# Performance work log

Measured on AMD Instinct MI355X. Metric: run time of the kernel, lower is better.

Reference implementation:

```python
import jax, jax.numpy as jnp
import numpy as np

N_LAYERS = 4


def setup_inputs() -> dict:
    key = jax.random.key(0)
    k1, k2 = jax.random.split(key)
    data = jax.random.normal(k1, (100000, 512), dtype=jnp.float32)
    codebooks = jax.random.normal(k2, (N_LAYERS, 1024, 512), dtype=jnp.float32) * 0.1
    return {"data": data, "codebooks": codebooks}


def _nearest(residual, cb):
    # squared euclidean distances [N, K]; argmin identical to cdist argmin
    x2 = jnp.sum(residual * residual, axis=1, keepdims=True)        # [N,1]
    c2 = jnp.sum(cb * cb, axis=1)[None, :]                          # [1,K]
    d2 = x2 + c2 - 2.0 * (residual @ cb.T)                          # [N,K]
    return jnp.argmin(d2, axis=1)


def reference(data, codebooks):
    """encode (iterative residual quantization) then decode. Returns (codes, reconstructed)."""
    residual = data
    codes = []
    recon = jnp.zeros_like(data)
    for l in range(N_LAYERS):  # small fixed layer count, sequential dependency
        cb = codebooks[l]                       # [K,F]
        idx = _nearest(residual, cb)            # [N]
        q = cb[idx]                             # gather [N,F]
        residual = residual - q
        recon = recon + q
        codes.append(idx)
    codes = jnp.stack(codes, axis=1).astype(jnp.int64)  # [N, n_layers]
    return codes, recon
```

## Files before the change

kernel.cpp:

```cpp
#include <hip/hip_runtime.h>
#include <hip/hip_bf16.h>
#include <math.h>

#define NL 4
#define KC 1024
#define FD 512
#define MT 32
#define BLK 512
#define HBLK 256
#define RS 516
#define PPS 132
#define NCAND 6

typedef __attribute__((ext_vector_type(8))) short short8;
typedef __attribute__((ext_vector_type(4))) float f32x4;

__device__ __forceinline__ short bf16c(float x) {
  __hip_bfloat16 h = __float2bfloat16(x);
  return *reinterpret_cast<short*>(&h);
}

__device__ __forceinline__ float np_chunk_partial(const float* p, int l16) {
  float pm[8];
#pragma unroll
  for (int m = 0; m < 8; m++) {
    float v = p[m * 16 + l16];
    pm[m] = __fmul_rn(v, v);
  }
  float a = __fadd_rn(__fadd_rn(pm[0], pm[1]), __fadd_rn(pm[2], pm[3]));
  float b = __fadd_rn(__fadd_rn(pm[4], pm[5]), __fadd_rn(pm[6], pm[7]));
  return __fadd_rn(a, b);
}

__global__ __launch_bounds__(HBLK) void c2_kernel(const float* __restrict__ cb,
                                                  float* __restrict__ c2) {
  int wid  = (blockIdx.x * HBLK + threadIdx.x) >> 6;
  int lane = threadIdx.x & 63;
  if (wid >= NL * KC) return;
  const float* row = cb + (size_t)wid * FD;
  int chunk = lane >> 4, l16 = lane & 15;
  float part = np_chunk_partial(row + chunk * 128, l16);
  part = __fadd_rn(part, __shfl_xor(part, 8));
  part = __fadd_rn(part, __shfl_xor(part, 4));
  part = __fadd_rn(part, __shfl_xor(part, 2));
  part = __fadd_rn(part, __shfl_xor(part, 1));
  float s1 = __fadd_rn(part, __shfl_xor(part, 16));
  float s  = __fadd_rn(s1, __shfl_xor(s1, 32));
  if (lane == 0) c2[wid] = s;
}

__global__ __launch_bounds__(HBLK) void swz_kernel(const float* __restrict__ cb,
                                                   short* __restrict__ cbw) {
  int g = blockIdx.x * HBLK + threadIdx.x;
  int w = g >> 6, lane = g & 63;
  if (w >= NL * 16 * 64) return;
  int l = w >> 10, c = (w >> 6) & 15, T = w & 63;
  int kidx = T * 16 + (lane & 15);
  int f0   = c * 32 + ((lane >> 4) << 3);
  const float* src = cb + (((size_t)l * KC + kidx) * FD + f0);
  short8 v;
#pragma unroll
  for (int j = 0; j < 8; j++) v[j] = bf16c(src[j]);
  *(short8*)(cbw + (size_t)w * 512 + lane * 8) = v;
}

#define INS(dval, kval) do {                                              \
    float _d = (dval); int _k = (kval);                                   \
    _Pragma("unroll")                                                     \
    for (int _j = 0; _j < NCAND; _j++) {                                  \
      bool _b = (_d < cd[_j]) || (_d == cd[_j] && _k < ck[_j]);           \
      if (_b) { float _td = cd[_j]; cd[_j] = _d; _d = _td;                \
                int   _tk = ck[_j]; ck[_j] = _k; _k = _tk; }              \
    }                                                                     \
  } while (0)

__global__ __launch_bounds__(BLK, 2) void rq_kernel(
    const float* __restrict__ data, const float* __restrict__ cb,
    const float* __restrict__ c2g, const short* __restrict__ cbw,
    float* __restrict__ codes_out, float* __restrict__ recon_out, int N) {
  __shared__ float resid[MT * RS];
  __shared__ float pool_d[MT * PPS];
  __shared__ int   pool_k[MT * PPS];
  __shared__ float mrg_d[MT * 24];
  __shared__ int   mrg_k[MT * 24];
  __shared__ float sh_part[MT * 64];
  __shared__ float sh_x2[MT];
  __shared__ float sc_d[MT * NCAND];
  __shared__ int   sc_k[MT * NCAND];
  __shared__ int   cand_k[MT * NCAND];
  __shared__ int   hist_k[NL * MT];

  const int t    = threadIdx.x;
  const int n0   = blockIdx.x * MT;
  if (n0 >= N) return;
  const int wv    = t >> 6;
  const int lane  = t & 63;
  const int l15   = lane & 15;
  const int lq    = lane >> 4;
  const int rh    = wv >> 2;
  const int wc    = wv & 3;
  const int rbase = rh << 4;

#pragma unroll
  for (int q = 0; q < 8; q++) {
    int id = t + BLK * q;
    int m = id >> 7, c4 = id & 127;
    int mg = n0 + m; if (mg > N - 1) mg = N - 1;
    *(float4*)&resid[m * RS + c4 * 4] =
        *(const float4*)&data[(size_t)mg * FD + c4 * 4];
  }
  __syncthreads();

  float4 rec[8];

  for (int l = 0; l < NL; l++) {
    const float* cbl = cb + (size_t)l * KC * FD;

    {
      int row = t >> 4, j16 = t & 15;
#pragma unroll
      for (int c = 0; c < 4; c++)
        sh_part[(row * 4 + c) * 16 + j16] =
            np_chunk_partial(&resid[row * RS + c * 128], j16);
    }
    __syncthreads();
    if (t < MT) {
      const float* P = &sh_part[t * 64];
      float b[4];
#pragma unroll
      for (int c = 0; c < 4; c++) {
        float u[8];
#pragma unroll
        for (int j2 = 0; j2 < 8; j2++)
          u[j2] = __fadd_rn(P[c * 16 + j2], P[c * 16 + j2 + 8]);
        float v[4];
#pragma unroll
        for (int j2 = 0; j2 < 4; j2++) v[j2] = __fadd_rn(u[j2], u[j2 + 4]);
        b[c] = __fadd_rn(__fadd_rn(v[0], v[2]), __fadd_rn(v[1], v[3]));
      }
      sh_x2[t] = __fadd_rn(__fadd_rn(b[0], b[1]), __fadd_rn(b[2], b[3]));
    }
    __syncthreads();

    f32x4 acc[16];
#pragma unroll
    for (int tt = 0; tt < 16; tt++) acc[tt] = (f32x4)0.f;

    float c2f[16];
#pragma unroll
    for (int tt = 0; tt < 16; tt++)
      c2f[tt] = c2g[l * KC + wc * 256 + tt * 16 + l15];

    for (int ch = 0; ch < 16; ch++) {
      float4 alo = *(const float4*)&resid[(rbase + l15) * RS + ch * 32 + lq * 8];
      float4 ahi = *(const float4*)&resid[(rbase + l15) * RS + ch * 32 + lq * 8 + 4];
      short8 av;
      av[0] = bf16c(alo.x); av[1] = bf16c(alo.y);
      av[2] = bf16c(alo.z); av[3] = bf16c(alo.w);
      av[4] = bf16c(ahi.x); av[5] = bf16c(ahi.y);
      av[6] = bf16c(ahi.z); av[7] = bf16c(ahi.w);
      const short8* bp =
          (const short8*)(cbw + (((size_t)l * 16 + ch) * 64 + wc * 16) * 512);
#pragma unroll
      for (int tt = 0; tt < 16; tt++) {
        short8 bv = bp[tt * 64 + lane];
        acc[tt] = __builtin_amdgcn_mfma_f32_16x16x32_bf16(av, bv, acc[tt],
                                                          0, 0, 0);
      }
    }

#pragma unroll
    for (int g = 0; g < 4; g++) {
      float b1 = INFINITY, b2 = INFINITY; int k1 = 0x7fffffff, k2 = 0x7fffffff;
#pragma unroll
      for (int tt = 0; tt < 16; tt++) {
        float s = c2f[tt] - 2.0f * acc[tt][g];
        int k = wc * 256 + tt * 16 + l15;
        if (s < b1) { b2 = b1; k2 = k1; b1 = s; k1 = k; }
        else if (s < b2) { b2 = s; k2 = k; }
      }
      int r = rbase + lq * 4 + g;
      int base = r * PPS + wc * 32 + l15 * 2;
      pool_d[base] = b1; pool_k[base] = k1;
      pool_d[base + 1] = b2; pool_k[base + 1] = k2;
    }
    __syncthreads();

    if (t < 4 * MT) {
      int r = t >> 2, seg = t & 3;
      const float4* pd4 = (const float4*)&pool_d[r * PPS + seg * 32];
      const int4*   pk4 = (const int4*)  &pool_k[r * PPS + seg * 32];
      float4 dv[8]; int4 kv[8];
#pragma unroll
      for (int e = 0; e < 8; e++) { dv[e] = pd4[e]; kv[e] = pk4[e]; }
      float cd[NCAND]; int ck[NCAND];
#pragma unroll
      for (int j = 0; j < NCAND; j++) { cd[j] = INFINITY; ck[j] = 0x7fffffff; }
#pragma unroll
      for (int e = 0; e < 8; e++) {
        INS(dv[e].x, kv[e].x); INS(dv[e].y, kv[e].y);
        INS(dv[e].z, kv[e].z); INS(dv[e].w, kv[e].w);
      }
#pragma unroll
      for (int j = 0; j < NCAND; j++) {
        mrg_d[r * 24 + seg * NCAND + j] = cd[j];
        mrg_k[r * 24 + seg * NCAND + j] = ck[j];
      }
    }
    __syncthreads();

    if (t < MT) {
      const float4* md4 = (const float4*)&mrg_d[t * 24];
      const int4*   mk4 = (const int4*)  &mrg_k[t * 24];
      float4 dv[6]; int4 kv[6];
#pragma unroll
      for (int e = 0; e < 6; e++) { dv[e] = md4[e]; kv[e] = mk4[e]; }
      float cd[NCAND]; int ck[NCAND];
#pragma unroll
      for (int j = 0; j < NCAND; j++) { cd[j] = INFINITY; ck[j] = 0x7fffffff; }
#pragma unroll
      for (int e = 0; e < 6; e++) {
        INS(dv[e].x, kv[e].x); INS(dv[e].y, kv[e].y);
        INS(dv[e].z, kv[e].z); INS(dv[e].w, kv[e].w);
      }
#pragma unroll
      for (int j = 0; j < NCAND; j++) cand_k[t * NCAND + j] = ck[j];
    }
    __syncthreads();

    if (t < MT * NCAND) {
      int r = t / NCAND, c = t - r * NCAND;
      int k = cand_k[r * NCAND + c];
      const float* cw = cbl + (size_t)k * FD;
      float sum = 0.f;
#pragma unroll 8
      for (int i = 0; i < 128; i++) {
        float4 rv = *(const float4*)&resid[r * RS + i * 4];
        float4 qv = *(const float4*)&cw[i * 4];
        sum = __fmaf_rn(rv.x, qv.x, sum);
        sum = __fmaf_rn(rv.y, qv.y, sum);
        sum = __fmaf_rn(rv.z, qv.z, sum);
        sum = __fmaf_rn(rv.w, qv.w, sum);
      }
      float c2e = c2g[l * KC + k];
      sc_d[r * NCAND + c] = __fsub_rn(__fadd_rn(sh_x2[r], c2e),
                                      __fmul_rn(2.0f, sum));
      sc_k[r * NCAND + c] = k;
    }
    __syncthreads();

    if (t < MT) {
      float bd = INFINITY; int bk = 0x7fffffff;
#pragma unroll
      for (int c = 0; c < NCAND; c++) {
        float d = sc_d[t * NCAND + c];
        int   k = sc_k[t * NCAND + c];
        if (d < bd || (d == bd && k < bk)) { bd = d; bk = k; }
      }
      hist_k[l * MT + t] = bk;
      if (n0 + t < N) codes_out[(size_t)(n0 + t) * NL + l] = (float)bk;
    }
    __syncthreads();

#pragma unroll
    for (int q = 0; q < 8; q++) {
      int id = t + BLK * q;
      int m = id >> 7, c4 = id & 127;
      int bk2 = hist_k[l * MT + m];
      float4 qv = *(const float4*)&cbl[(size_t)bk2 * FD + c4 * 4];
      if (l == 0) {
        rec[q] = qv;
      } else {
        rec[q].x = __fadd_rn(rec[q].x, qv.x);
        rec[q].y = __fadd_rn(rec[q].y, qv.y);
        rec[q].z = __fadd_rn(rec[q].z, qv.z);
        rec[q].w = __fadd_rn(rec[q].w, qv.w);
      }
      if (l < NL - 1) {
        float4 rv = *(float4*)&resid[m * RS + c4 * 4];
        rv.x = __fsub_rn(rv.x, qv.x); rv.y = __fsub_rn(rv.y, qv.y);
        rv.z = __fsub_rn(rv.z, qv.z); rv.w = __fsub_rn(rv.w, qv.w);
        *(float4*)&resid[m * RS + c4 * 4] = rv;
      }
    }
    if (l < NL - 1) __syncthreads();
  }

#pragma unroll
  for (int q = 0; q < 8; q++) {
    int id = t + BLK * q;
    int m = id >> 7, c4 = id & 127;
    int mg = n0 + m;
    if (mg < N)
      *(float4*)&recon_out[(size_t)mg * FD + c4 * 4] = rec[q];
  }
}

extern "C" void kernel_launch(void* const* d_in, const int* in_sizes, int n_in,
                              void* d_out, int out_size, void* d_ws, size_t ws_size,
                              hipStream_t stream) {
  const float* data = (const float*)d_in[0];
  const float* cb   = (const float*)d_in[1];
  int N = in_sizes[0] / FD;

  float* c2  = (float*)d_ws;
  short* cbw = (short*)((char*)d_ws + 16384);
  float* codes_out = (float*)d_out;
  float* recon_out = codes_out + (size_t)N * NL;

  c2_kernel<<<(NL * KC + 3) / 4, HBLK, 0, stream>>>(cb, c2);
  swz_kernel<<<(NL * 16 * 64) / 4, HBLK, 0, stream>>>(cb, cbw);
  int nblocks = (N + MT - 1) / MT;
  rq_kernel<<<nblocks, BLK, 0, stream>>>(data, cb, c2, cbw, codes_out,
                                         recon_out, N);
}
```

Before: 3.804 ms.

## Halve row tile to 16 rows per 256-thread block and shuffle-reduce norms

The main kernel now handles 16 rows per block with 4 waves, each covering a 256-code slice, instead of 32 rows with 8 waves. The squared-norm computation uses wave shuffles rather than a shared-memory partial buffer and an extra barrier. Occupancy is raised to 3 blocks per CU. Each codebook tile fetched from global/L2 is now reused across only 16 rows instead of 32, so codebook traffic per row doubles in exchange for smaller blocks and fewer syncs.

```diff
diff --git a/kernel.cpp b/kernel.cpp
--- a/kernel.cpp
+++ b/kernel.cpp
@@ -5,9 +5,8 @@
 #define NL 4
 #define KC 1024
 #define FD 512
-#define MT 32
-#define BLK 512
-#define HBLK 256
+#define MT 16
+#define BLK 256
 #define RS 516
 #define PPS 132
 #define NCAND 6
@@ -32,9 +31,9 @@
   return __fadd_rn(a, b);
 }
 
-__global__ __launch_bounds__(HBLK) void c2_kernel(const float* __restrict__ cb,
-                                                  float* __restrict__ c2) {
-  int wid  = (blockIdx.x * HBLK + threadIdx.x) >> 6;
+__global__ __launch_bounds__(BLK) void c2_kernel(const float* __restrict__ cb,
+                                                 float* __restrict__ c2) {
+  int wid  = (blockIdx.x * BLK + threadIdx.x) >> 6;
   int lane = threadIdx.x & 63;
   if (wid >= NL * KC) return;
   const float* row = cb + (size_t)wid * FD;
@@ -49,9 +48,9 @@
   if (lane == 0) c2[wid] = s;
 }
 
-__global__ __launch_bounds__(HBLK) void swz_kernel(const float* __restrict__ cb,
-                                                   short* __restrict__ cbw) {
-  int g = blockIdx.x * HBLK + threadIdx.x;
+__global__ __launch_bounds__(BLK) void swz_kernel(const float* __restrict__ cb,
+                                                  short* __restrict__ cbw) {
+  int g = blockIdx.x * BLK + threadIdx.x;
   int w = g >> 6, lane = g & 63;
   if (w >= NL * 16 * 64) return;
   int l = w >> 10, c = (w >> 6) & 15, T = w & 63;
@@ -74,7 +73,7 @@
     }                                                                     \
   } while (0)
 
-__global__ __launch_bounds__(BLK, 2) void rq_kernel(
+__global__ __launch_bounds__(BLK, 3) void rq_kernel(
     const float* __restrict__ data, const float* __restrict__ cb,
     const float* __restrict__ c2g, const short* __restrict__ cbw,
     float* __restrict__ codes_out, float* __restrict__ recon_out, int N) {
@@ -83,7 +82,6 @@
   __shared__ int   pool_k[MT * PPS];
   __shared__ float mrg_d[MT * 24];
   __shared__ int   mrg_k[MT * 24];
-  __shared__ float sh_part[MT * 64];
   __shared__ float sh_x2[MT];
   __shared__ float sc_d[MT * NCAND];
   __shared__ int   sc_k[MT * NCAND];
@@ -93,13 +91,10 @@
   const int t    = threadIdx.x;
   const int n0   = blockIdx.x * MT;
   if (n0 >= N) return;
-  const int wv    = t >> 6;
-  const int lane  = t & 63;
-  const int l15   = lane & 15;
-  const int lq    = lane >> 4;
-  const int rh    = wv >> 2;
-  const int wc    = wv & 3;
-  const int rbase = rh << 4;
+  const int wv   = t >> 6;
+  const int lane = t & 63;
+  const int l15  = lane & 15;
+  const int lq   = lane >> 4;
 
 #pragma unroll
   for (int q = 0; q < 8; q++) {
@@ -117,30 +112,19 @@
     const float* cbl = cb + (size_t)l * KC * FD;
 
     {
-      int row = t >> 4, j16 = t & 15;
-#pragma unroll
-      for (int c = 0; c < 4; c++)
-        sh_part[(row * 4 + c) * 16 + j16] =
-            np_chunk_partial(&resid[row * RS + c * 128], j16);
-    }
-    __syncthreads();
-    if (t < MT) {
-      const float* P = &sh_part[t * 64];
+      int row = wv * 4 + lq;
       float b[4];
 #pragma unroll
       for (int c = 0; c < 4; c++) {
-        float u[8];
-#pragma unroll
-        for (int j2 = 0; j2 < 8; j2++)
-          u[j2] = __fadd_rn(P[c * 16 + j2], P[c * 16 + j2 + 8]);
-        float v[4];
-#pragma unroll
-        for (int j2 = 0; j2 < 4; j2++) v[j2] = __fadd_rn(u[j2], u[j2 + 4]);
-        b[c] = __fadd_rn(__fadd_rn(v[0], v[2]), __fadd_rn(v[1], v[3]));
-      }
-      sh_x2[t] = __fadd_rn(__fadd_rn(b[0], b[1]), __fadd_rn(b[2], b[3]));
-    }
-    __syncthreads();
+        float part = np_chunk_partial(&resid[row * RS + c * 128], l15);
+        float u = __fadd_rn(part, __shfl_xor(part, 8));
+        float v = __fadd_rn(u, __shfl_xor(u, 4));
+        float w = __fadd_rn(v, __shfl_xor(v, 2));
+        b[c] = __fadd_rn(w, __shfl_xor(w, 1));
+      }
+      if (l15 == 0)
+        sh_x2[row] = __fadd_rn(__fadd_rn(b[0], b[1]), __fadd_rn(b[2], b[3]));
+    }
 
     f32x4 acc[16];
 #pragma unroll
@@ -149,18 +133,18 @@
     float c2f[16];
 #pragma unroll
     for (int tt = 0; tt < 16; tt++)
-      c2f[tt] = c2g[l * KC + wc * 256 + tt * 16 + l15];
+      c2f[tt] = c2g[l * KC + wv * 256 + tt * 16 + l15];
 
     for (int ch = 0; ch < 16; ch++) {
-      float4 alo = *(const float4*)&resid[(rbase + l15) * RS + ch * 32 + lq * 8];
-      float4 ahi = *(const float4*)&resid[(rbase + l15) * RS + ch * 32 + lq * 8 + 4];
+      float4 alo = *(const float4*)&resid[l15 * RS + ch * 32 + lq * 8];
+      float4 ahi = *(const float4*)&resid[l15 * RS + ch * 32 + lq * 8 + 4];
       short8 av;
       av[0] = bf16c(alo.x); av[1] = bf16c(alo.y);
       av[2] = bf16c(alo.z); av[3] = bf16c(alo.w);
       av[4] = bf16c(ahi.x); av[5] = bf16c(ahi.y);
       av[6] = bf16c(ahi.z); av[7] = bf16c(ahi.w);
       const short8* bp =
-          (const short8*)(cbw + (((size_t)l * 16 + ch) * 64 + wc * 16) * 512);
+          (const short8*)(cbw + (((size_t)l * 16 + ch) * 64 + wv * 16) * 512);
 #pragma unroll
       for (int tt = 0; tt < 16; tt++) {
         short8 bv = bp[tt * 64 + lane];
@@ -175,12 +159,12 @@
 #pragma unroll
       for (int tt = 0; tt < 16; tt++) {
         float s = c2f[tt] - 2.0f * acc[tt][g];
-        int k = wc * 256 + tt * 16 + l15;
+        int k = wv * 256 + tt * 16 + l15;
         if (s < b1) { b2 = b1; k2 = k1; b1 = s; k1 = k; }
         else if (s < b2) { b2 = s; k2 = k; }
       }
-      int r = rbase + lq * 4 + g;
-      int base = r * PPS + wc * 32 + l15 * 2;
+      int r = lq * 4 + g;
+      int base = r * PPS + wv * 32 + l15 * 2;
       pool_d[base] = b1; pool_k[base] = k1;
       pool_d[base + 1] = b2; pool_k[base + 1] = k2;
     }
@@ -308,8 +292,8 @@
   float* codes_out = (float*)d_out;
   float* recon_out = codes_out + (size_t)N * NL;
 
-  c2_kernel<<<(NL * KC + 3) / 4, HBLK, 0, stream>>>(cb, c2);
-  swz_kernel<<<(NL * 16 * 64) / 4, HBLK, 0, stream>>>(cb, cbw);
+  c2_kernel<<<(NL * KC + 3) / 4, BLK, 0, stream>>>(cb, c2);
+  swz_kernel<<<(NL * 16 * 64) / 4, BLK, 0, stream>>>(cb, cbw);
   int nblocks = (N + MT - 1) / MT;
   rq_kernel<<<nblocks, BLK, 0, stream>>>(data, cb, c2, cbw, codes_out,
                                          recon_out, N);
```

Measured after the change: 5.618 ms. 1.48x slower.
